# Performance work log

Measured on AMD Instinct MI355X. Metric: run time of the kernel, lower is better.

## Reference

```python
import jax, jax.numpy as jnp
import numpy as np

D_MODEL = 1024
NUM_HEADS = 16
HEAD_DIM = D_MODEL // NUM_HEADS


def setup_inputs() -> dict:
    key = jax.random.key(0)
    ks = jax.random.split(key, 11)
    B, S = 2, 2048
    s = 1.0 / np.sqrt(D_MODEL)
    inp = {
        "query": jax.random.normal(ks[0], (B, S, D_MODEL), jnp.float32),
        "key": jax.random.normal(ks[1], (B, S, D_MODEL), jnp.float32),
        "value": jax.random.normal(ks[2], (B, S, D_MODEL), jnp.float32),
        "Wq": jax.random.normal(ks[3], (D_MODEL, D_MODEL), jnp.float32) * s,
        "bq": jnp.zeros((D_MODEL,), jnp.float32),
        "Wk": jax.random.normal(ks[4], (D_MODEL, D_MODEL), jnp.float32) * s,
        "bk": jnp.zeros((D_MODEL,), jnp.float32),
        "Wv": jax.random.normal(ks[5], (D_MODEL, D_MODEL), jnp.float32) * s,
        "bv": jnp.zeros((D_MODEL,), jnp.float32),
        "Wo": jax.random.normal(ks[6], (D_MODEL, D_MODEL), jnp.float32) * s,
        "bo": jnp.zeros((D_MODEL,), jnp.float32),
    }
    return inp


def _split_heads(x):
    B, S, _ = x.shape
    return x.reshape(B, S, NUM_HEADS, HEAD_DIM).transpose(0, 2, 1, 3)  # [B,H,S,d]


def reference(query, key, value, Wq, bq, Wk, bk, Wv, bv, Wo, bo):
    Q = _split_heads(query @ Wq.T + bq)
    K = _split_heads(key @ Wk.T + bk)
    V = _split_heads(value @ Wv.T + bv)
    scale = 1.0 / jnp.sqrt(jnp.asarray(HEAD_DIM, jnp.float32))
    scores = jnp.einsum("bhqd,bhkd->bhqk", Q, K) * scale  # [B,H,S,S]
    weights = jax.nn.softmax(scores, axis=-1)
    attn = jnp.einsum("bhqk,bhkd->bhqd", weights, V)
    B, H, S, d = attn.shape
    attn = attn.transpose(0, 2, 1, 3).reshape(B, S, H * d)
    return attn @ Wo.T + bo
```

## Files before the change

### kernel.cpp

```cpp
#include <hip/hip_runtime.h>
#include <hip/hip_bf16.h>


typedef unsigned short u16;
typedef __attribute__((ext_vector_type(8))) short short8;
typedef __attribute__((ext_vector_type(4))) float floatx4;

__device__ __forceinline__ float bf2f(u16 x) {
  return __uint_as_float(((unsigned)x) << 16);
}
__device__ __forceinline__ u16 f2bf(float f) {
  unsigned x = __float_as_uint(f);
  return (u16)((x + 0x7fffu + ((x >> 16) & 1u)) >> 16);
}
__device__ __forceinline__ ushort2 pk_bf16(float a, float b) {
  __hip_bfloat162 h2 = __float22bfloat162_rn(make_float2(a, b));
  ushort2 u;
  __builtin_memcpy(&u, &h2, 4);
  return u;
}
#if __has_builtin(__builtin_amdgcn_exp2f)
#define EXP2(x) __builtin_amdgcn_exp2f(x)
#else
#define EXP2(x) exp2f(x)
#endif
__device__ __forceinline__ void gll16(const u16* g, u16* lds) {
  __builtin_amdgcn_global_load_lds((const __attribute__((address_space(1))) void*)g,
                                   (__attribute__((address_space(3))) void*)lds,
                                   16, 0, 0);
}
#define DSFENCE() __asm__ volatile("s_waitcnt lgkmcnt(0)" ::: "memory")

__global__ __launch_bounds__(256) void cvt_kernel(
    const float* __restrict__ q, const float* __restrict__ k, const float* __restrict__ v,
    const float* __restrict__ wq, const float* __restrict__ wk,
    const float* __restrict__ wv, const float* __restrict__ wo,
    const float* __restrict__ bq, const float* __restrict__ bk,
    const float* __restrict__ bv, const float* __restrict__ bo,
    u16* __restrict__ ws) {
  const int i4 = (blockIdx.x * 256 + threadIdx.x) * 4;
  const float* src;
  u16* dst;
  int local;
  if (i4 < 4194304)        { src = q;  dst = ws;            local = i4; }
  else if (i4 < 8388608)   { src = k;  dst = ws + 4194304;  local = i4 - 4194304; }
  else if (i4 < 12582912)  { src = v;  dst = ws + 8388608;  local = i4 - 8388608; }
  else if (i4 < 13631488)  { src = wq; dst = ws + 12582912; local = i4 - 12582912; }
  else if (i4 < 14680064)  { src = wk; dst = ws + 13631488; local = i4 - 13631488; }
  else if (i4 < 15728640)  { src = wv; dst = ws + 14680064; local = i4 - 14680064; }
  else if (i4 < 16777216)  { src = wo; dst = ws + 15728640; local = i4 - 15728640; }
  else if (i4 < 16778240)  { src = bq; dst = ws + 16777216; local = i4 - 16777216; }
  else if (i4 < 16779264)  { src = bk; dst = ws + 16779264; local = i4 - 16778240; }
  else if (i4 < 16780288)  { src = bv; dst = ws + 16781312; local = i4 - 16779264; }
  else                     { src = bo; dst = ws + 16783360; local = i4 - 16780288; }
  const float4 f = *(const float4*)(src + local);
  ushort4 o;
  o.x = f2bf(f.x); o.y = f2bf(f.y); o.z = f2bf(f.z); o.w = f2bf(f.w);
  *(ushort4*)(dst + local) = o;
}

__device__ __forceinline__ void gemm_tile(
    const u16* __restrict__ X, const u16* __restrict__ W,
    const u16* __restrict__ bias, u16* __restrict__ out16, float* __restrict__ out32,
    int row0, int col0, int mode, float oscale, u16* As, u16* Bs) {
  const int tid = threadIdx.x;
  const int w = tid >> 6, l = tid & 63;
  const int lan = l & 15, quad = l >> 4;
  const int wm = w & 1, wn = w >> 1;

  floatx4 acc[4][4];
#pragma unroll
  for (int i = 0; i < 4; ++i)
#pragma unroll
    for (int j = 0; j < 4; ++j) acc[i][j] = (floatx4)0.0f;

  const int r0 = tid >> 2, kq0 = tid & 3;
  const int r1 = (tid + 256) >> 2;
  u16* aB0 = As + w * 512;
  u16* aB1 = As + 2048 + w * 512;
  u16* bB0 = Bs + w * 512;
  u16* bB1 = Bs + 2048 + w * 512;
  const u16* Xa0 = X + (size_t)(row0 + r0) * 1024 + kq0 * 8;
  const u16* Xa1 = X + (size_t)(row0 + r1) * 1024 + kq0 * 8;
  const u16* Wb0 = W + (size_t)(col0 + r0) * 1024 + kq0 * 8;
  const u16* Wb1 = W + (size_t)(col0 + r1) * 1024 + kq0 * 8;

  for (int kt = 0; kt < 32; ++kt) {
    gll16(Xa0 + kt * 32, aB0);
    gll16(Xa1 + kt * 32, aB1);
    gll16(Wb0 + kt * 32, bB0);
    gll16(Wb1 + kt * 32, bB1);
    __syncthreads();

    short8 af[4], bfr[4];
#pragma unroll
    for (int i = 0; i < 4; ++i)
      af[i] = *(const short8*)(As + (wm * 64 + i * 16 + lan) * 32 + quad * 8);
#pragma unroll
    for (int j = 0; j < 4; ++j)
      bfr[j] = *(const short8*)(Bs + (wn * 64 + j * 16 + lan) * 32 + quad * 8);
#pragma unroll
    for (int i = 0; i < 4; ++i)
#pragma unroll
      for (int j = 0; j < 4; ++j)
        acc[i][j] = __builtin_amdgcn_mfma_f32_16x16x32_bf16(af[i], bfr[j], acc[i][j], 0, 0, 0);
    __syncthreads();
  }

#pragma unroll
  for (int i = 0; i < 4; ++i) {
    const int mb = row0 + wm * 64 + i * 16 + quad * 4;
#pragma unroll
    for (int j = 0; j < 4; ++j) {
      const int n = col0 + wn * 64 + j * 16 + lan;
      const float bv = bf2f(bias[n]);
      if (mode == 0) {
#pragma unroll
        for (int r = 0; r < 4; ++r)
          out16[(size_t)(mb + r) * 1024 + n] = f2bf((acc[i][j][r] + bv) * oscale);
      } else if (mode == 1) {
        const int b = mb >> 11;
        const int h = n >> 6, dd = n & 63;
        u16* base = out16 + (size_t)((b * 16 + h) * 64 + dd) * 2048;
#pragma unroll
        for (int r = 0; r < 4; ++r) {
          const int s = (mb + r) & 2047;
          const int sp = (s & ~63) | ((s & 15) * 4 + ((s >> 4) & 3));
          base[sp] = f2bf(acc[i][j][r] + bv);
        }
      } else {
#pragma unroll
        for (int r = 0; r < 4; ++r)
          out32[(size_t)(mb + r) * 1024 + n] = acc[i][j][r] + bv;
      }
    }
  }
}

__global__ __launch_bounds__(256) void qkv_kernel(
    const u16* __restrict__ xq, const u16* __restrict__ xk, const u16* __restrict__ xv,
    const u16* __restrict__ Wq, const u16* __restrict__ Wk, const u16* __restrict__ Wv,
    const u16* __restrict__ bq, const u16* __restrict__ bk, const u16* __restrict__ bv,
    u16* __restrict__ Qo, u16* __restrict__ Ko, u16* __restrict__ Vto) {
  __shared__ __align__(16) u16 As[128 * 32];
  __shared__ __align__(16) u16 Bs[128 * 32];
  const int bx = blockIdx.x;
  const int tile_m = bx / 24;
  const int rem = bx - tile_m * 24;
  const int which = rem >> 3;
  const int col0 = (rem & 7) * 128;
  const u16* X = which == 0 ? xq : (which == 1 ? xk : xv);
  const u16* W = which == 0 ? Wq : (which == 1 ? Wk : Wv);
  const u16* bias = which == 0 ? bq : (which == 1 ? bk : bv);
  u16* out = which == 0 ? Qo : (which == 1 ? Ko : Vto);
  const float C = 0.125f * 1.4426950408889634f;
  gemm_tile(X, W, bias, out, nullptr, tile_m * 128, col0, which == 2 ? 1 : 0,
            which == 0 ? C : 1.0f, As, Bs);
}

__global__ __launch_bounds__(256) void proj_kernel(
    const u16* __restrict__ X, const u16* __restrict__ W,
    const u16* __restrict__ bias, float* __restrict__ out) {
  __shared__ __align__(16) u16 As[128 * 32];
  __shared__ __align__(16) u16 Bs[128 * 32];
  const int bx = blockIdx.x;
  gemm_tile(X, W, bias, nullptr, out, (bx >> 3) * 128, (bx & 7) * 128, 2, 1.0f, As, Bs);
}

#define FIXMAX 16.0f
#define KPAD 72
__global__ __launch_bounds__(256, 2) void attn_kernel(
    const u16* __restrict__ Q, const u16* __restrict__ K,
    const u16* __restrict__ Vt, u16* __restrict__ O) {
  __shared__ __align__(16) u16 Ks[64 * KPAD];
  __shared__ __align__(16) u16 Vs[64 * KPAD];
  __shared__ __align__(16) u16 Ps[128 * KPAD];
  const int tid = threadIdx.x;
  const int w = tid >> 6, l = tid & 63;
  const int lan = l & 15, quad = l >> 4;
  const int q0 = blockIdx.x * 128;
  const int bh = blockIdx.y;
  const int b = bh >> 4, h = bh & 15;
  const u16* Qg = Q + (size_t)(b * 2048 + q0) * 1024 + h * 64;
  const u16* Kg = K + (size_t)(b * 2048) * 1024 + h * 64;
  const u16* Vg = Vt + (size_t)((b * 16 + h) * 64) * 2048;

  short8 aq[2][2];
#pragma unroll
  for (int mi = 0; mi < 2; ++mi)
#pragma unroll
    for (int kk = 0; kk < 2; ++kk)
      aq[mi][kk] = *(const short8*)(Qg + (size_t)(w * 32 + mi * 16 + lan) * 1024 +
                                    kk * 32 + quad * 8);

  float lrun[2][4];
  floatx4 oacc[2][4];
#pragma unroll
  for (int mi = 0; mi < 2; ++mi) {
#pragma unroll
    for (int r = 0; r < 4; ++r) lrun[mi][r] = 0.f;
#pragma unroll
    for (int nd = 0; nd < 4; ++nd) oacc[mi][nd] = (floatx4)0.0f;
  }

  const int rowA = tid >> 3, colq = (tid & 7) * 8;
  const int rowB = rowA + 32;

  short8 k0 = *(const short8*)(Kg + (size_t)rowA * 1024 + colq);
  short8 k1 = *(const short8*)(Kg + (size_t)rowB * 1024 + colq);
  short8 v0 = *(const short8*)(Vg + (size_t)rowA * 2048 + colq);
  short8 v1 = *(const short8*)(Vg + (size_t)rowB * 2048 + colq);

  for (int kt = 0; kt < 32; ++kt) {
    __syncthreads();
    *(short8*)(Ks + rowA * KPAD + colq) = k0;
    *(short8*)(Ks + rowB * KPAD + colq) = k1;
    *(short8*)(Vs + rowA * KPAD + colq) = v0;
    *(short8*)(Vs + rowB * KPAD + colq) = v1;
    __syncthreads();

    const int kn = kt < 31 ? kt + 1 : 31;
    k0 = *(const short8*)(Kg + (size_t)(kn * 64 + rowA) * 1024 + colq);
    k1 = *(const short8*)(Kg + (size_t)(kn * 64 + rowB) * 1024 + colq);
    v0 = *(const short8*)(Vg + (size_t)rowA * 2048 + kn * 64 + colq);
    v1 = *(const short8*)(Vg + (size_t)rowB * 2048 + kn * 64 + colq);

    short8 bkf[4][2];
#pragma unroll
    for (int nj = 0; nj < 4; ++nj)
#pragma unroll
      for (int kk = 0; kk < 2; ++kk)
        bkf[nj][kk] = *(const short8*)(Ks + (nj * 16 + lan) * KPAD + kk * 32 + quad * 8);

    floatx4 sacc[2][4];
#pragma unroll
    for (int mi = 0; mi < 2; ++mi)
#pragma unroll
      for (int nj = 0; nj < 4; ++nj) sacc[mi][nj] = (floatx4)(-FIXMAX);
#pragma unroll
    for (int kk = 0; kk < 2; ++kk)
#pragma unroll
      for (int mi = 0; mi < 2; ++mi)
#pragma unroll
        for (int nj = 0; nj < 4; ++nj)
          sacc[mi][nj] =
              __builtin_amdgcn_mfma_f32_16x16x32_bf16(aq[mi][kk], bkf[nj][kk], sacc[mi][nj], 0, 0, 0);

#pragma unroll
    for (int mi = 0; mi < 2; ++mi)
#pragma unroll
      for (int r = 0; r < 4; ++r) {
        const float p0 = EXP2(sacc[mi][0][r]), p1 = EXP2(sacc[mi][1][r]);
        const float p2 = EXP2(sacc[mi][2][r]), p3 = EXP2(sacc[mi][3][r]);
        lrun[mi][r] += (p0 + p1) + (p2 + p3);
        const ushort2 a01 = pk_bf16(p0, p1);
        const ushort2 a23 = pk_bf16(p2, p3);
        ushort4 pp;
        pp.x = a01.x; pp.y = a01.y; pp.z = a23.x; pp.w = a23.y;
        const int qrow = w * 32 + mi * 16 + quad * 4 + r;
        *(ushort4*)(Ps + qrow * KPAD + lan * 4) = pp;
      }
    DSFENCE();

    short8 pa[2][2];
#pragma unroll
    for (int mi = 0; mi < 2; ++mi)
#pragma unroll
      for (int kk = 0; kk < 2; ++kk)
        pa[mi][kk] = *(const short8*)(Ps + (w * 32 + mi * 16 + lan) * KPAD + kk * 32 + quad * 8);
    short8 vb[4][2];
#pragma unroll
    for (int nd = 0; nd < 4; ++nd)
#pragma unroll
      for (int kk = 0; kk < 2; ++kk)
        vb[nd][kk] = *(const short8*)(Vs + (nd * 16 + lan) * KPAD + kk * 32 + quad * 8);
#pragma unroll
    for (int kk = 0; kk < 2; ++kk)
#pragma unroll
      for (int mi = 0; mi < 2; ++mi)
#pragma unroll
        for (int nd = 0; nd < 4; ++nd)
          oacc[mi][nd] =
              __builtin_amdgcn_mfma_f32_16x16x32_bf16(pa[mi][kk], vb[nd][kk], oacc[mi][nd], 0, 0, 0);
  }

#pragma unroll
  for (int mi = 0; mi < 2; ++mi)
#pragma unroll
    for (int r = 0; r < 4; ++r) {
      float ls = lrun[mi][r];
#pragma unroll
      for (int d = 1; d < 16; d <<= 1) ls += __shfl_xor(ls, d);
      const float inv = 1.0f / ls;
      const int mg = b * 2048 + q0 + w * 32 + mi * 16 + quad * 4 + r;
#pragma unroll
      for (int nd = 0; nd < 4; ++nd) {
        const int col = h * 64 + nd * 16 + lan;
        O[(size_t)mg * 1024 + col] = f2bf(oacc[mi][nd][r] * inv);
      }
    }
}

extern "C" void kernel_launch(void* const* d_in, const int* in_sizes, int n_in,
                              void* d_out, int out_size, void* d_ws, size_t ws_size,
                              hipStream_t stream) {
  const float* query = (const float*)d_in[0];
  const float* key_ = (const float*)d_in[1];
  const float* value = (const float*)d_in[2];
  const float* Wq = (const float*)d_in[3];
  const float* bq = (const float*)d_in[4];
  const float* Wk = (const float*)d_in[5];
  const float* bk = (const float*)d_in[6];
  const float* Wv = (const float*)d_in[7];
  const float* bv = (const float*)d_in[8];
  const float* Wo = (const float*)d_in[9];
  const float* bo = (const float*)d_in[10];
  float* out = (float*)d_out;

  u16* ws = (u16*)d_ws;
  u16* Xq = ws;
  u16* Xk = ws + 4194304;
  u16* Xv = ws + 8388608;
  u16* cWq = ws + 12582912;
  u16* cWk = ws + 13631488;
  u16* cWv = ws + 14680064;
  u16* cWo = ws + 15728640;
  u16* cbq = ws + 16777216;
  u16* cbk = ws + 16779264;
  u16* cbv = ws + 16781312;
  u16* cbo = ws + 16783360;
  u16* Qw = ws + 17301504;
  u16* Kw = ws + 21495808;
  u16* Vtw = ws + 25690112;
  u16* Ow = ws + 29884416;

  cvt_kernel<<<16388, 256, 0, stream>>>(query, key_, value, Wq, Wk, Wv, Wo,
                                        bq, bk, bv, bo, ws);
  qkv_kernel<<<768, 256, 0, stream>>>(Xq, Xk, Xv, cWq, cWk, cWv, cbq, cbk, cbv,
                                      Qw, Kw, Vtw);
  attn_kernel<<<dim3(16, 32), 256, 0, stream>>>(Qw, Kw, Vtw, Ow);
  proj_kernel<<<256, 256, 0, stream>>>(Ow, cWo, cbo, out);
}
```

Baseline: 237.6 us.

## Triple-buffer GEMM LDS staging and double-buffer K/V tiles in attention

The GEMM tile loop now keeps three LDS stages in flight. Direct-to-LDS loads are issued two iterations ahead and gated with explicit vmcnt waits and raw barriers, replacing the two __syncthreads per iteration. The attention kernel double-buffers its K/V LDS tiles so each iteration needs one barrier. It also hoists the V fragment reads ahead of the P fence and raises wave priority around MFMA blocks. LDS use rises (48KB per GEMM block, more in attention), which may reduce occupancy.

```diff
diff --git a/kernel.cpp b/kernel.cpp
--- a/kernel.cpp
+++ b/kernel.cpp
@@ -76,36 +76,55 @@
 
   const int r0 = tid >> 2, kq0 = tid & 3;
   const int r1 = (tid + 256) >> 2;
-  u16* aB0 = As + w * 512;
-  u16* aB1 = As + 2048 + w * 512;
-  u16* bB0 = Bs + w * 512;
-  u16* bB1 = Bs + 2048 + w * 512;
+  const int woff = w * 512;
   const u16* Xa0 = X + (size_t)(row0 + r0) * 1024 + kq0 * 8;
   const u16* Xa1 = X + (size_t)(row0 + r1) * 1024 + kq0 * 8;
   const u16* Wb0 = W + (size_t)(col0 + r0) * 1024 + kq0 * 8;
   const u16* Wb1 = W + (size_t)(col0 + r1) * 1024 + kq0 * 8;
 
+#define STAGE(buf, kt)                                         \
+  do {                                                         \
+    gll16(Xa0 + (kt) * 32, As + (buf) * 4096 + woff);          \
+    gll16(Xa1 + (kt) * 32, As + (buf) * 4096 + 2048 + woff);   \
+    gll16(Wb0 + (kt) * 32, Bs + (buf) * 4096 + woff);          \
+    gll16(Wb1 + (kt) * 32, Bs + (buf) * 4096 + 2048 + woff);   \
+  } while (0)
+
+  STAGE(0, 0);
+  STAGE(1, 1);
+  int cur = 0;
   for (int kt = 0; kt < 32; ++kt) {
-    gll16(Xa0 + kt * 32, aB0);
-    gll16(Xa1 + kt * 32, aB1);
-    gll16(Wb0 + kt * 32, bB0);
-    gll16(Wb1 + kt * 32, bB1);
-    __syncthreads();
-
+    if (kt < 30) {
+      const int nb = cur == 0 ? 2 : cur - 1;
+      STAGE(nb, kt + 2);
+      __asm__ volatile("s_waitcnt vmcnt(8)" ::: "memory");
+    } else if (kt == 30) {
+      __asm__ volatile("s_waitcnt vmcnt(4)" ::: "memory");
+    } else {
+      __asm__ volatile("s_waitcnt vmcnt(0)" ::: "memory");
+    }
+    __builtin_amdgcn_s_barrier();
+
+    const u16* Ab = As + cur * 4096;
+    const u16* Bb = Bs + cur * 4096;
     short8 af[4], bfr[4];
 #pragma unroll
     for (int i = 0; i < 4; ++i)
-      af[i] = *(const short8*)(As + (wm * 64 + i * 16 + lan) * 32 + quad * 8);
+      af[i] = *(const short8*)(Ab + (wm * 64 + i * 16 + lan) * 32 + quad * 8);
 #pragma unroll
     for (int j = 0; j < 4; ++j)
-      bfr[j] = *(const short8*)(Bs + (wn * 64 + j * 16 + lan) * 32 + quad * 8);
+      bfr[j] = *(const short8*)(Bb + (wn * 64 + j * 16 + lan) * 32 + quad * 8);
+    __asm__ volatile("s_waitcnt lgkmcnt(0)" ::: "memory");
+    __builtin_amdgcn_s_barrier();
+
 #pragma unroll
     for (int i = 0; i < 4; ++i)
 #pragma unroll
       for (int j = 0; j < 4; ++j)
         acc[i][j] = __builtin_amdgcn_mfma_f32_16x16x32_bf16(af[i], bfr[j], acc[i][j], 0, 0, 0);
-    __syncthreads();
+    cur = cur == 2 ? 0 : cur + 1;
   }
+#undef STAGE
 
 #pragma unroll
   for (int i = 0; i < 4; ++i) {
@@ -142,8 +161,8 @@
     const u16* __restrict__ Wq, const u16* __restrict__ Wk, const u16* __restrict__ Wv,
     const u16* __restrict__ bq, const u16* __restrict__ bk, const u16* __restrict__ bv,
     u16* __restrict__ Qo, u16* __restrict__ Ko, u16* __restrict__ Vto) {
-  __shared__ __align__(16) u16 As[128 * 32];
-  __shared__ __align__(16) u16 Bs[128 * 32];
+  __shared__ __align__(16) u16 As[3 * 4096];
+  __shared__ __align__(16) u16 Bs[3 * 4096];
   const int bx = blockIdx.x;
   const int tile_m = bx / 24;
   const int rem = bx - tile_m * 24;
@@ -161,8 +180,8 @@
 __global__ __launch_bounds__(256) void proj_kernel(
     const u16* __restrict__ X, const u16* __restrict__ W,
     const u16* __restrict__ bias, float* __restrict__ out) {
-  __shared__ __align__(16) u16 As[128 * 32];
-  __shared__ __align__(16) u16 Bs[128 * 32];
+  __shared__ __align__(16) u16 As[3 * 4096];
+  __shared__ __align__(16) u16 Bs[3 * 4096];
   const int bx = blockIdx.x;
   gemm_tile(X, W, bias, nullptr, out, (bx >> 3) * 128, (bx & 7) * 128, 2, 1.0f, As, Bs);
 }
@@ -172,8 +191,8 @@
 __global__ __launch_bounds__(256, 2) void attn_kernel(
     const u16* __restrict__ Q, const u16* __restrict__ K,
     const u16* __restrict__ Vt, u16* __restrict__ O) {
-  __shared__ __align__(16) u16 Ks[64 * KPAD];
-  __shared__ __align__(16) u16 Vs[64 * KPAD];
+  __shared__ __align__(16) u16 Ks[2][64 * KPAD];
+  __shared__ __align__(16) u16 Vs[2][64 * KPAD];
   __shared__ __align__(16) u16 Ps[128 * KPAD];
   const int tid = threadIdx.x;
   const int w = tid >> 6, l = tid & 63;
@@ -210,33 +229,37 @@
   short8 k1 = *(const short8*)(Kg + (size_t)rowB * 1024 + colq);
   short8 v0 = *(const short8*)(Vg + (size_t)rowA * 2048 + colq);
   short8 v1 = *(const short8*)(Vg + (size_t)rowB * 2048 + colq);
+  *(short8*)(Ks[0] + rowA * KPAD + colq) = k0;
+  *(short8*)(Ks[0] + rowB * KPAD + colq) = k1;
+  *(short8*)(Vs[0] + rowA * KPAD + colq) = v0;
+  *(short8*)(Vs[0] + rowB * KPAD + colq) = v1;
+  __syncthreads();
 
   for (int kt = 0; kt < 32; ++kt) {
-    __syncthreads();
-    *(short8*)(Ks + rowA * KPAD + colq) = k0;
-    *(short8*)(Ks + rowB * KPAD + colq) = k1;
-    *(short8*)(Vs + rowA * KPAD + colq) = v0;
-    *(short8*)(Vs + rowB * KPAD + colq) = v1;
-    __syncthreads();
-
-    const int kn = kt < 31 ? kt + 1 : 31;
-    k0 = *(const short8*)(Kg + (size_t)(kn * 64 + rowA) * 1024 + colq);
-    k1 = *(const short8*)(Kg + (size_t)(kn * 64 + rowB) * 1024 + colq);
-    v0 = *(const short8*)(Vg + (size_t)rowA * 2048 + kn * 64 + colq);
-    v1 = *(const short8*)(Vg + (size_t)rowB * 2048 + kn * 64 + colq);
+    const int cur = kt & 1;
+    if (kt < 31) {
+      const int kn = kt + 1;
+      k0 = *(const short8*)(Kg + (size_t)(kn * 64 + rowA) * 1024 + colq);
+      k1 = *(const short8*)(Kg + (size_t)(kn * 64 + rowB) * 1024 + colq);
+      v0 = *(const short8*)(Vg + (size_t)rowA * 2048 + kn * 64 + colq);
+      v1 = *(const short8*)(Vg + (size_t)rowB * 2048 + kn * 64 + colq);
+    }
+    const u16* Kc = Ks[cur];
+    const u16* Vc = Vs[cur];
 
     short8 bkf[4][2];
 #pragma unroll
     for (int nj = 0; nj < 4; ++nj)
 #pragma unroll
       for (int kk = 0; kk < 2; ++kk)
-        bkf[nj][kk] = *(const short8*)(Ks + (nj * 16 + lan) * KPAD + kk * 32 + quad * 8);
+        bkf[nj][kk] = *(const short8*)(Kc + (nj * 16 + lan) * KPAD + kk * 32 + quad * 8);
 
     floatx4 sacc[2][4];
 #pragma unroll
     for (int mi = 0; mi < 2; ++mi)
 #pragma unroll
       for (int nj = 0; nj < 4; ++nj) sacc[mi][nj] = (floatx4)(-FIXMAX);
+    __builtin_amdgcn_s_setprio(1);
 #pragma unroll
     for (int kk = 0; kk < 2; ++kk)
 #pragma unroll
@@ -245,6 +268,7 @@
         for (int nj = 0; nj < 4; ++nj)
           sacc[mi][nj] =
               __builtin_amdgcn_mfma_f32_16x16x32_bf16(aq[mi][kk], bkf[nj][kk], sacc[mi][nj], 0, 0, 0);
+    __builtin_amdgcn_s_setprio(0);
 
 #pragma unroll
     for (int mi = 0; mi < 2; ++mi)
@@ -260,6 +284,13 @@
         const int qrow = w * 32 + mi * 16 + quad * 4 + r;
         *(ushort4*)(Ps + qrow * KPAD + lan * 4) = pp;
       }
+
+    short8 vb[4][2];
+#pragma unroll
+    for (int nd = 0; nd < 4; ++nd)
+#pragma unroll
+      for (int kk = 0; kk < 2; ++kk)
+        vb[nd][kk] = *(const short8*)(Vc + (nd * 16 + lan) * KPAD + kk * 32 + quad * 8);
     DSFENCE();
 
     short8 pa[2][2];
@@ -268,12 +299,7 @@
 #pragma unroll
       for (int kk = 0; kk < 2; ++kk)
         pa[mi][kk] = *(const short8*)(Ps + (w * 32 + mi * 16 + lan) * KPAD + kk * 32 + quad * 8);
-    short8 vb[4][2];
-#pragma unroll
-    for (int nd = 0; nd < 4; ++nd)
-#pragma unroll
-      for (int kk = 0; kk < 2; ++kk)
-        vb[nd][kk] = *(const short8*)(Vs + (nd * 16 + lan) * KPAD + kk * 32 + quad * 8);
+    __builtin_amdgcn_s_setprio(1);
 #pragma unroll
     for (int kk = 0; kk < 2; ++kk)
 #pragma unroll
@@ -282,6 +308,17 @@
         for (int nd = 0; nd < 4; ++nd)
           oacc[mi][nd] =
               __builtin_amdgcn_mfma_f32_16x16x32_bf16(pa[mi][kk], vb[nd][kk], oacc[mi][nd], 0, 0, 0);
+    __builtin_amdgcn_s_setprio(0);
+
+    if (kt < 31) {
+      u16* Kn = Ks[cur ^ 1];
+      u16* Vn = Vs[cur ^ 1];
+      *(short8*)(Kn + rowA * KPAD + colq) = k0;
+      *(short8*)(Kn + rowB * KPAD + colq) = k1;
+      *(short8*)(Vn + rowA * KPAD + colq) = v0;
+      *(short8*)(Vn + rowB * KPAD + colq) = v1;
+      __syncthreads();
+    }
   }
 
 #pragma unroll
```

Result: no change. 238.6 us (+0.4%).
